# Optimization experiments

Measured on AMD Instinct MI355X. Metric: run time of the kernel, lower is better.

Reference implementation:

```python
import jax, jax.numpy as jnp
import numpy as np

PAD = 0

def setup_inputs() -> dict:
    key = jax.random.key(0)
    ks = jax.random.split(key, 16)
    B, S, D, F = 64, 512, 768, 256
    VOCAB = 32000
    # variable-length tweets: length in [8, S], rest is padding (token id PAD=0)
    lengths = jax.random.randint(ks[0], (B,), 8, S + 1)
    tok = jax.random.randint(ks[1], (B, S), 1, VOCAB)
    x = jnp.where(jnp.arange(S)[None, :] < lengths[:, None], tok, PAD)
    h = jax.random.normal(ks[2], (B, S, D), dtype=jnp.float32)
    sc = 0.02
    w2 = jax.random.normal(ks[3], (F, D, 2), dtype=jnp.float32) * sc
    b2 = jax.random.normal(ks[4], (F,), dtype=jnp.float32) * sc
    w3 = jax.random.normal(ks[5], (F, D, 3), dtype=jnp.float32) * sc
    b3 = jax.random.normal(ks[6], (F,), dtype=jnp.float32) * sc
    w4 = jax.random.normal(ks[7], (F, D, 4), dtype=jnp.float32) * sc
    b4 = jax.random.normal(ks[8], (F,), dtype=jnp.float32) * sc
    w5 = jax.random.normal(ks[9], (F, D, 5), dtype=jnp.float32) * sc
    b5 = jax.random.normal(ks[10], (F,), dtype=jnp.float32) * sc
    fc_w = jax.random.normal(ks[11], (1, 4 * F), dtype=jnp.float32) * sc
    fc_b = jax.random.normal(ks[12], (1,), dtype=jnp.float32) * sc
    return {"x": x, "h": h, "w2": w2, "b2": b2, "w3": w3, "b3": b3,
            "w4": w4, "b4": b4, "w5": w5, "b5": b5, "fc_w": fc_w, "fc_b": fc_b}


def _branch(hc, L, w, b):
    # hc: [B, D, S] front-compacted hidden states; w: [F, D, k]
    k = w.shape[-1]
    out = jax.lax.conv_general_dilated(
        hc, w, window_strides=(1,), padding='VALID',
        dimension_numbers=('NCH', 'OIH', 'NCH')) + b[None, :, None]  # [B,F,S-k+1]
    T = out.shape[-1]
    # conv position t is valid iff t + k - 1 < L  <=>  t < L - k + 1
    valid = jnp.arange(T)[None, :] < (L - k + 1)[:, None]           # [B,T]
    neg = jnp.asarray(-jnp.inf, out.dtype)
    pooled = jnp.max(jnp.where(valid[:, None, :], out, neg), axis=-1)  # [B,F]
    return jax.nn.relu(pooled)


def reference(x, h, w2, b2, w3, b3, w4, b4, w5, b5, fc_w, fc_b):
    mask = x != PAD                                   # [B,S]
    L = mask.sum(axis=1)                              # [B]
    # stable compaction: move non-pad token hidden states to the front, order preserved
    order = jnp.argsort(jnp.logical_not(mask), axis=1, stable=True)   # [B,S]
    hc = jnp.take_along_axis(h, order[..., None], axis=1)             # [B,S,D]
    hc = hc.transpose(0, 2, 1)                                        # [B,D,S]
    feats = jnp.concatenate([
        _branch(hc, L, w2, b2),
        _branch(hc, L, w3, b3),
        _branch(hc, L, w4, b4),
        _branch(hc, L, w5, b5),
    ], axis=-1)                                       # [B, 4F]
    logits = feats @ fc_w.T + fc_b                    # [B,1]
    return jax.nn.sigmoid(logits).squeeze(-1)         # [B]
```

## Files before the change

kernel.cpp:

```cpp
#include <hip/hip_runtime.h>
#include <stdint.h>

#define Bn 64
#define Sn 512
#define SPn 520
#define Dn 768
#define JSTRIDE 196608
#define ABUF 16640
#define BSLOT 8192
#define QS_A 28.222222f
#define SAQ 0.035433072f

typedef int iv4 __attribute__((ext_vector_type(4)));

static __device__ __forceinline__ signed char q8(float f, float s) {
  float t = __builtin_rintf(f * s);
  t = fmaxf(-127.f, fminf(127.f, t));
  return (signed char)(int)t;
}

static __device__ __forceinline__ void gload16(const void* g, void* l) {
  __builtin_amdgcn_global_load_lds(
      (const __attribute__((address_space(1))) unsigned int*)g,
      (__attribute__((address_space(3))) unsigned int*)l, 16, 0, 0);
}

template<int N> __device__ __forceinline__ void waitv() {
  static_assert(N == 0 || N == 1 || N == 4, "");
  if constexpr (N == 0) asm volatile("s_waitcnt vmcnt(0)" ::: "memory");
  else if constexpr (N == 1) asm volatile("s_waitcnt vmcnt(1)" ::: "memory");
  else asm volatile("s_waitcnt vmcnt(4)" ::: "memory");
}

__global__ __launch_bounds__(256) void plan_kernel(
    const int* __restrict__ x, int* __restrict__ plan, int* __restrict__ rowmap) {
  __shared__ int sL[64];
  __shared__ int sOff[65];
  int tid = threadIdx.x, lane = tid & 63, wv = tid >> 6;
  for (int bb = wv; bb < 64; bb += 4) {
    int cnt = 0;
    for (int c = 0; c < 8; ++c) {
      unsigned long long m = __ballot(x[bb * Sn + c * 64 + lane] != 0);
      cnt += __popcll(m);
    }
    if (lane == 0) sL[bb] = cnt;
  }
  __syncthreads();
  if (tid < 64) {
    int L = sL[tid];
    int SL = (L + 15) & ~15;
    int pre = SL;
    #pragma unroll
    for (int off = 1; off < 64; off <<= 1) {
      int y = __shfl_up(pre, off);
      if (tid >= off) pre += y;
    }
    sOff[tid] = pre - SL;
    if (tid == 63) { sOff[64] = pre; plan[0] = (pre + 255) >> 8; }
  }
  __syncthreads();
  int M = sOff[64];
  for (int b = 0; b < 64; ++b) {
    int off = sOff[b], L = sL[b];
    int SL = (L + 15) & ~15;
    int enc = (b << 20) | (L << 10);
    for (int t = tid; t < SL; t += 256) rowmap[off + t] = enc | t;
  }
  for (int p = M + tid; p < M + 264; p += 256)
    rowmap[p] = 512;
}

__global__ __launch_bounds__(256) void stage_kernel(
    const int* __restrict__ x, const float* __restrict__ h,
    const float* __restrict__ w2, const float* __restrict__ w3,
    const float* __restrict__ w4, const float* __restrict__ w5,
    signed char* __restrict__ hcq, signed char* __restrict__ wq,
    float* __restrict__ fscale) {
  int tid = threadIdx.x, lane = tid & 63, wv = tid >> 6;
  if (blockIdx.x < 512) {
    int cidx = blockIdx.x;
    int b = cidx >> 3, rblk = cidx & 7;
    __shared__ unsigned long long masks[8];
    __shared__ short sidx[Sn];
    for (int c = wv; c < 8; c += 4) {
      unsigned long long m = __ballot(x[b * Sn + c * 64 + lane] != 0);
      if (lane == 0) masks[c] = m;
    }
    __syncthreads();
    int pref[9]; pref[0] = 0;
    #pragma unroll
    for (int c = 0; c < 8; ++c) pref[c + 1] = pref[c] + __popcll(masks[c]);
    int L = pref[8];
    for (int p = tid; p < Sn; p += 256) {
      int c = p >> 6, l = p & 63;
      unsigned long long m = masks[c];
      if ((m >> l) & 1ull)
        sidx[pref[c] + __popcll(m & ((1ull << l) - 1ull))] = (short)p;
    }
    __syncthreads();
    int r0 = rblk * 65;
    for (int r = r0 + wv; r < r0 + 65; r += 4) {
      if (r < L) {
        signed char* dst = hcq + ((size_t)b * SPn + r) * Dn;
        const float* src = h + ((size_t)b * Sn + sidx[r]) * Dn;
        #pragma unroll
        for (int c = 0; c < 3; ++c) {
          int d = c * 256 + lane * 4;
          float4 v = *(const float4*)(src + d);
          char4 o = { q8(v.x, QS_A), q8(v.y, QS_A), q8(v.z, QS_A), q8(v.w, QS_A) };
          *(char4*)(dst + d) = o;
        }
      }
    }
  } else {
    __shared__ float sf[3840];
    __shared__ float smax[4];
    int bb = blockIdx.x - 512;
    int br = bb >> 8, f = bb & 255, k = br + 2;
    const float* w = (br == 0) ? w2 : (br == 1) ? w3 : (br == 2) ? w4 : w5;
    int mBase = 256 * ((br * (br + 3)) >> 1);
    const float* src = w + (size_t)f * Dn * k;
    int n = Dn * k;
    float mx = 0.f;
    for (int e = tid; e < n; e += 256) {
      float v = src[e];
      sf[e] = v;
      mx = fmaxf(mx, fabsf(v));
    }
    #pragma unroll
    for (int off = 32; off; off >>= 1) mx = fmaxf(mx, __shfl_xor(mx, off));
    if (lane == 0) smax[wv] = mx;
    __syncthreads();
    float M = fmaxf(fmaxf(smax[0], smax[1]), fmaxf(smax[2], smax[3]));
    M = fmaxf(M, 1e-30f);
    if (tid == 0) fscale[br * 256 + f] = M / 127.f;
    float qs = 127.f / M;
    for (int j = 0; j < k; ++j) {
      signed char* dst = wq + (size_t)(mBase + j * 256 + f) * Dn;
      for (int d = tid; d < Dn; d += 256) dst[d] = q8(sf[d * k + j], qs);
    }
  }
}

static __device__ __forceinline__ void issueA(
    int d0i, char* sA, const char* const (&gA)[2], const char* gAt,
    int lane, int wvoff) {
  int aoff = (d0i + 1) * 64;
  char* nA = sA + ((d0i + 1) & 1) * ABUF;
  #pragma unroll
  for (int p = 0; p < 2; ++p) gload16(gA[p] + aoff, nA + p * 8192 + wvoff);
  if (lane < 16) gload16(gAt + aoff, nA + 16384);
}

template<int J, int W, int J2, int DADD, int DOA>
static __device__ __forceinline__ void conv_step(
    int d0i, int bsl0, char* sA, char* sB,
    const char* const (&gA)[2], const char* gAt, const char* gB0,
    int lane, int wr, int wc, int lrow, int lg, int wvoff, iv4 (&acc)[4][4]) {
  int sl = bsl0 + J;      sl  -= (sl  >= 3) ? 3 : 0; sl  -= (sl  >= 3) ? 3 : 0;
  int dsl = bsl0 + J + 2; dsl -= (dsl >= 3) ? 3 : 0; dsl -= (dsl >= 3) ? 3 : 0;
  {
    int boff = J2 * JSTRIDE + (d0i + DADD) * 64;
    gload16(gB0 + boff, sB + dsl * BSLOT + wvoff);
  }
  if constexpr (DOA) issueA(d0i, sA, gA, gAt, lane, wvoff);
  const char* curA = sA + (d0i & 1) * ABUF;
  const char* curB = sB + sl * BSLOT;
  iv4 Af[4], Bf[4];
  #pragma unroll
  for (int m = 0; m < 4; ++m) {
    int row = wr * 64 + m * 16 + lrow + J;
    Af[m] = *(const iv4*)(curA + row * 64 + ((lg ^ ((row >> 1) & 3)) << 4));
  }
  #pragma unroll
  for (int n = 0; n < 4; ++n) {
    int row = wc * 64 + n * 16 + lrow;
    Bf[n] = *(const iv4*)(curB + row * 64 + ((lg ^ ((row >> 1) & 3)) << 4));
  }
  __builtin_amdgcn_s_setprio(1);
  #pragma unroll
  for (int n = 0; n < 4; ++n)
    #pragma unroll
    for (int m = 0; m < 4; ++m)
      acc[m][n] = __builtin_amdgcn_mfma_i32_16x16x64_i8(Af[m], Bf[n], acc[m][n], 0, 0, 0);
  __builtin_amdgcn_s_setprio(0);
  __builtin_amdgcn_sched_barrier(0);
  waitv<W>();
  __builtin_amdgcn_sched_barrier(0);
  __builtin_amdgcn_s_barrier();
  __builtin_amdgcn_sched_barrier(0);
}

#define SA bsl0, sA, sB, gA, gAt, gB0, lane, wr, wc, lrow, lg, wvoff, acc

template<int KK>
static __device__ __forceinline__ void conv_loop(
    char* sA, char* sB, const char* const (&gA)[2], const char* gAt,
    const char* gB0,
    int lane, int wr, int wc, int lrow, int lg, int wvoff, iv4 (&acc)[4][4]) {
  #pragma unroll
  for (int p = 0; p < 2; ++p) gload16(gA[p], sA + p * 8192 + wvoff);
  if (lane < 16) gload16(gAt, sA + 16384);
  gload16(gB0, sB + wvoff);
  gload16(gB0 + JSTRIDE, sB + BSLOT + wvoff);
  __builtin_amdgcn_sched_barrier(0);
  waitv<1>();
  __builtin_amdgcn_sched_barrier(0);
  __builtin_amdgcn_s_barrier();
  __builtin_amdgcn_sched_barrier(0);
  int bsl0 = 0;
  for (int d0i = 0; d0i < 11; ++d0i) {
    if constexpr (KK == 5) {
      conv_step<0,4,2,0,1>(d0i, SA);
      conv_step<1,4,3,0,0>(d0i, SA);
      conv_step<2,1,4,0,0>(d0i, SA);
      conv_step<3,1,0,1,0>(d0i, SA);
      conv_step<4,1,1,1,0>(d0i, SA);
    } else if constexpr (KK == 4) {
      conv_step<0,4,2,0,1>(d0i, SA);
      conv_step<1,4,3,0,0>(d0i, SA);
      conv_step<2,1,0,1,0>(d0i, SA);
      conv_step<3,1,1,1,0>(d0i, SA);
    } else if constexpr (KK == 3) {
      conv_step<0,4,2,0,1>(d0i, SA);
      conv_step<1,4,0,1,0>(d0i, SA);
      conv_step<2,1,1,1,0>(d0i, SA);
    } else {
      conv_step<0,4,0,1,1>(d0i, SA);
      conv_step<1,1,1,1,0>(d0i, SA);
    }
    bsl0 += KK; bsl0 -= (bsl0 >= 3) ? 3 : 0; bsl0 -= (bsl0 >= 3) ? 3 : 0;
  }
  if constexpr (KK == 5) {
    conv_step<0,1,2,0,0>(11, SA);
    conv_step<1,1,3,0,0>(11, SA);
    conv_step<2,1,4,0,0>(11, SA);
    conv_step<3,1,0,1,0>(11, SA);
    conv_step<4,1,1,1,0>(11, SA);
  } else if constexpr (KK == 4) {
    conv_step<0,1,2,0,0>(11, SA);
    conv_step<1,1,3,0,0>(11, SA);
    conv_step<2,1,0,1,0>(11, SA);
    conv_step<3,1,1,1,0>(11, SA);
  } else if constexpr (KK == 3) {
    conv_step<0,1,2,0,0>(11, SA);
    conv_step<1,1,0,1,0>(11, SA);
    conv_step<2,1,1,1,0>(11, SA);
  } else {
    conv_step<0,1,0,1,0>(11, SA);
    conv_step<1,1,1,1,0>(11, SA);
  }
  waitv<0>();
}

__global__ __launch_bounds__(512, 4) void conv_kernel(
    const signed char* __restrict__ hcq, const signed char* __restrict__ wq,
    const float* __restrict__ b2, const float* __restrict__ b3,
    const float* __restrict__ b4, const float* __restrict__ b5,
    const float* __restrict__ fscale,
    const int* __restrict__ plan, const int* __restrict__ rowmap,
    int* __restrict__ feats) {
  __shared__ char smem[2 * ABUF + 3 * BSLOT];
  char* sA = smem;
  char* sB = smem + 2 * ABUF;
  int idx = blockIdx.x;
  int xcd = idx & 7, s2 = idx >> 3;
  int sub = s2 & 7, tile = xcd + ((s2 >> 3) << 3);
  if (tile >= plan[0]) return;
  int br = 3 - (sub >> 1), ff = sub & 1, kk = br + 2;
  int mBase = 256 * ((br * (br + 3)) >> 1) + ff * 128;
  const float* bias = (br == 0) ? b2 : (br == 1) ? b3 : (br == 2) ? b4 : b5;
  int tid = threadIdx.x, lane = tid & 63, wv = tid >> 6;
  int wr = wv >> 1, wc = wv & 1;
  int lrow = lane & 15, lg = lane >> 4;
  int wvoff = wv * 1024;
  int P0 = tile << 8;

  const char* gA[2];
  #pragma unroll
  for (int p = 0; p < 2; ++p) {
    int c = p * 512 + tid;
    int row = c >> 2, sgp = c & 3;
    int rm = rowmap[P0 + row];
    int bb_ = rm >> 20, t = rm & 1023;
    int seg = sgp ^ ((row >> 1) & 3);
    gA[p] = (const char*)(hcq + ((size_t)(bb_ * SPn + t)) * Dn + seg * 16);
  }
  const char* gAt;
  {
    int l = lane & 15;
    int row = 256 + (l >> 2), sgp = l & 3;
    int rm = rowmap[P0 + row];
    int bb_ = rm >> 20, t = rm & 1023;
    int seg = sgp ^ ((row >> 1) & 3);
    gAt = (const char*)(hcq + ((size_t)(bb_ * SPn + t)) * Dn + seg * 16);
  }
  const char* gB0;
  {
    int row = tid >> 2, sgp = tid & 3;
    int seg = sgp ^ ((row >> 1) & 3);
    gB0 = (const char*)(wq + ((size_t)(mBase + row)) * Dn + seg * 16);
  }

  iv4 acc[4][4];
  #pragma unroll
  for (int m = 0; m < 4; ++m)
    #pragma unroll
    for (int n = 0; n < 4; ++n) acc[m][n] = (iv4)0;

  switch (br) {
    case 3: conv_loop<5>(sA, sB, gA, gAt, gB0, lane, wr, wc, lrow, lg, wvoff, acc); break;
    case 2: conv_loop<4>(sA, sB, gA, gAt, gB0, lane, wr, wc, lrow, lg, wvoff, acc); break;
    case 1: conv_loop<3>(sA, sB, gA, gAt, gB0, lane, wr, wc, lrow, lg, wvoff, acc); break;
    default: conv_loop<2>(sA, sB, gA, gAt, gB0, lane, wr, wc, lrow, lg, wvoff, acc); break;
  }

  int rmv[4];
  #pragma unroll
  for (int m = 0; m < 4; ++m) rmv[m] = rowmap[P0 + wr * 64 + m * 16];
  #pragma unroll
  for (int n = 0; n < 4; ++n) {
    int fg = ff * 128 + wc * 64 + n * 16 + lrow;
    float bv = bias[fg];
    float sfc = fscale[br * 256 + fg] * SAQ;
    #pragma unroll
    for (int m = 0; m < 4; ++m) {
      int bb_ = rmv[m] >> 20;
      int Lb = (rmv[m] >> 10) & 1023;
      int t0 = (rmv[m] & 1023) + lg * 4;
      int vlim = Lb - kk + 1;
      float pmax = 0.f;
      #pragma unroll
      for (int i = 0; i < 4; ++i) {
        float v = (float)acc[m][n][i] * sfc + bv;
        pmax = fmaxf(pmax, (t0 + i < vlim) ? fmaxf(v, 0.f) : 0.f);
      }
      pmax = fmaxf(pmax, __shfl_xor(pmax, 16));
      pmax = fmaxf(pmax, __shfl_xor(pmax, 32));
      if (lane < 16 && pmax > 0.f)
        atomicMax(feats + bb_ * 1024 + br * 256 + fg, __float_as_int(pmax));
    }
  }
}

__global__ __launch_bounds__(64) void fc_kernel(
    const int* __restrict__ feats, const float* __restrict__ fcw,
    const float* __restrict__ fcb, float* __restrict__ out) {
  int b = blockIdx.x, lane = threadIdx.x;
  float acc = 0.f;
  for (int i = lane; i < 1024; i += 64)
    acc += __int_as_float(feats[b * 1024 + i]) * fcw[i];
  #pragma unroll
  for (int off = 32; off; off >>= 1) acc += __shfl_xor(acc, off);
  if (lane == 0) out[b] = 1.f / (1.f + expf(-(acc + fcb[0])));
}

extern "C" void kernel_launch(void* const* d_in, const int* in_sizes, int n_in,
                              void* d_out, int out_size, void* d_ws, size_t ws_size,
                              hipStream_t stream) {
  const int*   x   = (const int*)d_in[0];
  const float* h   = (const float*)d_in[1];
  const float* w2  = (const float*)d_in[2];
  const float* b2  = (const float*)d_in[3];
  const float* w3  = (const float*)d_in[4];
  const float* b3  = (const float*)d_in[5];
  const float* w4  = (const float*)d_in[6];
  const float* b4  = (const float*)d_in[7];
  const float* w5  = (const float*)d_in[8];
  const float* b5  = (const float*)d_in[9];
  const float* fcw = (const float*)d_in[10];
  const float* fcb = (const float*)d_in[11];
  float* out = (float*)d_out;
  char* ws = (char*)d_ws;
  signed char* hcq = (signed char*)ws;
  signed char* wq  = (signed char*)(ws + 25559040);
  float* fscale = (float*)(ws + 28311552);
  int* feats  = (int*)(ws + 28315648);
  int* plan   = (int*)(ws + 28577792);
  int* rowmap = (int*)(ws + 28577808);

  hipMemsetAsync(feats, 0, 64 * 1024 * 4, stream);
  plan_kernel<<<1, 256, 0, stream>>>(x, plan, rowmap);
  stage_kernel<<<1536, 256, 0, stream>>>(x, h, w2, w3, w4, w5, hcq, wq, fscale);
  conv_kernel<<<1024, 512, 0, stream>>>(hcq, wq, b2, b3, b4, b5, fscale, plan, rowmap, feats);
  fc_kernel<<<64, 64, 0, stream>>>(feats, fcw, fcb, out);
}
```

Measured before the change: 115.2 us.

## Stage all conv taps per depth chunk with double buffering, fold memset into plan kernel

Replaces the per-tap fine-grained pipeline (three rotating B slots, one barrier per tap, explicit vmcnt waits) with a coarser double-buffered scheme. Each depth chunk now loads all KK weight taps plus the activation tile, then computes every tap, with one __syncthreads per chunk. This cuts barrier count, but LDS grows to roughly 115KB per block and the occupancy hint is dropped, so fewer blocks fit per CU and the prefetch relies on the compiler's implicit waits. It also zeroes feats inside plan_kernel instead of calling hipMemsetAsync, and vectorizes the weight-quantization stores to char4.

After: 110.0 us. 4.5% less time.

```diff
diff --git a/kernel.cpp b/kernel.cpp
--- a/kernel.cpp
+++ b/kernel.cpp
@@ -25,18 +25,16 @@
       (__attribute__((address_space(3))) unsigned int*)l, 16, 0, 0);
 }
 
-template<int N> __device__ __forceinline__ void waitv() {
-  static_assert(N == 0 || N == 1 || N == 4, "");
-  if constexpr (N == 0) asm volatile("s_waitcnt vmcnt(0)" ::: "memory");
-  else if constexpr (N == 1) asm volatile("s_waitcnt vmcnt(1)" ::: "memory");
-  else asm volatile("s_waitcnt vmcnt(4)" ::: "memory");
-}
-
 __global__ __launch_bounds__(256) void plan_kernel(
-    const int* __restrict__ x, int* __restrict__ plan, int* __restrict__ rowmap) {
+    const int* __restrict__ x, int* __restrict__ plan, int* __restrict__ rowmap,
+    int* __restrict__ feats) {
   __shared__ int sL[64];
   __shared__ int sOff[65];
   int tid = threadIdx.x, lane = tid & 63, wv = tid >> 6;
+  {
+    int4 z = {0, 0, 0, 0};
+    for (int i = tid * 4; i < 65536; i += 1024) *(int4*)(feats + i) = z;
+  }
   for (int bb = wv; bb < 64; bb += 4) {
     int cnt = 0;
     for (int c = 0; c < 8; ++c) {
@@ -137,130 +135,86 @@
     float qs = 127.f / M;
     for (int j = 0; j < k; ++j) {
       signed char* dst = wq + (size_t)(mBase + j * 256 + f) * Dn;
-      for (int d = tid; d < Dn; d += 256) dst[d] = q8(sf[d * k + j], qs);
-    }
-  }
-}
-
-static __device__ __forceinline__ void issueA(
-    int d0i, char* sA, const char* const (&gA)[2], const char* gAt,
-    int lane, int wvoff) {
-  int aoff = (d0i + 1) * 64;
-  char* nA = sA + ((d0i + 1) & 1) * ABUF;
-  #pragma unroll
-  for (int p = 0; p < 2; ++p) gload16(gA[p] + aoff, nA + p * 8192 + wvoff);
-  if (lane < 16) gload16(gAt + aoff, nA + 16384);
-}
-
-template<int J, int W, int J2, int DADD, int DOA>
-static __device__ __forceinline__ void conv_step(
-    int d0i, int bsl0, char* sA, char* sB,
-    const char* const (&gA)[2], const char* gAt, const char* gB0,
-    int lane, int wr, int wc, int lrow, int lg, int wvoff, iv4 (&acc)[4][4]) {
-  int sl = bsl0 + J;      sl  -= (sl  >= 3) ? 3 : 0; sl  -= (sl  >= 3) ? 3 : 0;
-  int dsl = bsl0 + J + 2; dsl -= (dsl >= 3) ? 3 : 0; dsl -= (dsl >= 3) ? 3 : 0;
-  {
-    int boff = J2 * JSTRIDE + (d0i + DADD) * 64;
-    gload16(gB0 + boff, sB + dsl * BSLOT + wvoff);
-  }
-  if constexpr (DOA) issueA(d0i, sA, gA, gAt, lane, wvoff);
-  const char* curA = sA + (d0i & 1) * ABUF;
-  const char* curB = sB + sl * BSLOT;
-  iv4 Af[4], Bf[4];
-  #pragma unroll
-  for (int m = 0; m < 4; ++m) {
-    int row = wr * 64 + m * 16 + lrow + J;
-    Af[m] = *(const iv4*)(curA + row * 64 + ((lg ^ ((row >> 1) & 3)) << 4));
-  }
-  #pragma unroll
-  for (int n = 0; n < 4; ++n) {
-    int row = wc * 64 + n * 16 + lrow;
-    Bf[n] = *(const iv4*)(curB + row * 64 + ((lg ^ ((row >> 1) & 3)) << 4));
-  }
-  __builtin_amdgcn_s_setprio(1);
-  #pragma unroll
-  for (int n = 0; n < 4; ++n)
-    #pragma unroll
-    for (int m = 0; m < 4; ++m)
-      acc[m][n] = __builtin_amdgcn_mfma_i32_16x16x64_i8(Af[m], Bf[n], acc[m][n], 0, 0, 0);
-  __builtin_amdgcn_s_setprio(0);
-  __builtin_amdgcn_sched_barrier(0);
-  waitv<W>();
-  __builtin_amdgcn_sched_barrier(0);
-  __builtin_amdgcn_s_barrier();
-  __builtin_amdgcn_sched_barrier(0);
-}
-
-#define SA bsl0, sA, sB, gA, gAt, gB0, lane, wr, wc, lrow, lg, wvoff, acc
+      for (int d4 = tid * 4; d4 < Dn; d4 += 1024) {
+        char4 o = { q8(sf[(d4 + 0) * k + j], qs), q8(sf[(d4 + 1) * k + j], qs),
+                    q8(sf[(d4 + 2) * k + j], qs), q8(sf[(d4 + 3) * k + j], qs) };
+        *(char4*)(dst + d4) = o;
+      }
+    }
+  }
+}
+
+template<int KK>
+static __device__ __forceinline__ void stageAll(
+    int d0, char* sA, char* sB, const char* const (&gA)[2], const char* gAt,
+    const char* gB0, int lane, int wvoff) {
+  int buf = d0 & 1;
+  char* bB = sB + buf * (KK * BSLOT);
+  int doff = d0 * 64;
+  #pragma unroll
+  for (int tap = 0; tap < KK; ++tap)
+    gload16(gB0 + tap * JSTRIDE + doff, bB + tap * BSLOT + wvoff);
+  char* nA = sA + buf * ABUF;
+  gload16(gA[0] + doff, nA + wvoff);
+  gload16(gA[1] + doff, nA + 8192 + wvoff);
+  if (lane < 16) gload16(gAt + doff, nA + 16384);
+}
+
+template<int KK>
+static __device__ __forceinline__ void computeD0(
+    int d0, const char* sA, const char* sB, int wr, int wc, int lrow, int lg,
+    iv4 (&acc)[4][4]) {
+  int buf = d0 & 1;
+  const char* curA = sA + buf * ABUF;
+  const char* bB = sB + buf * (KK * BSLOT);
+  #pragma unroll
+  for (int j = 0; j < KK; ++j) {
+    const char* curB = bB + j * BSLOT;
+    iv4 Af[4], Bf[4];
+    #pragma unroll
+    for (int n = 0; n < 4; ++n) {
+      int row = wc * 64 + n * 16 + lrow;
+      Bf[n] = *(const iv4*)(curB + row * 64 + ((lg ^ ((row >> 1) & 3)) << 4));
+    }
+    #pragma unroll
+    for (int m = 0; m < 4; ++m) {
+      int row = wr * 64 + m * 16 + lrow + j;
+      Af[m] = *(const iv4*)(curA + row * 64 + ((lg ^ ((row >> 1) & 3)) << 4));
+    }
+    __builtin_amdgcn_s_setprio(1);
+    #pragma unroll
+    for (int n = 0; n < 4; ++n)
+      #pragma unroll
+      for (int m = 0; m < 4; ++m)
+        acc[m][n] = __builtin_amdgcn_mfma_i32_16x16x64_i8(Af[m], Bf[n], acc[m][n], 0, 0, 0);
+    __builtin_amdgcn_s_setprio(0);
+  }
+}
 
 template<int KK>
 static __device__ __forceinline__ void conv_loop(
     char* sA, char* sB, const char* const (&gA)[2], const char* gAt,
-    const char* gB0,
-    int lane, int wr, int wc, int lrow, int lg, int wvoff, iv4 (&acc)[4][4]) {
-  #pragma unroll
-  for (int p = 0; p < 2; ++p) gload16(gA[p], sA + p * 8192 + wvoff);
-  if (lane < 16) gload16(gAt, sA + 16384);
-  gload16(gB0, sB + wvoff);
-  gload16(gB0 + JSTRIDE, sB + BSLOT + wvoff);
-  __builtin_amdgcn_sched_barrier(0);
-  waitv<1>();
-  __builtin_amdgcn_sched_barrier(0);
-  __builtin_amdgcn_s_barrier();
-  __builtin_amdgcn_sched_barrier(0);
-  int bsl0 = 0;
-  for (int d0i = 0; d0i < 11; ++d0i) {
-    if constexpr (KK == 5) {
-      conv_step<0,4,2,0,1>(d0i, SA);
-      conv_step<1,4,3,0,0>(d0i, SA);
-      conv_step<2,1,4,0,0>(d0i, SA);
-      conv_step<3,1,0,1,0>(d0i, SA);
-      conv_step<4,1,1,1,0>(d0i, SA);
-    } else if constexpr (KK == 4) {
-      conv_step<0,4,2,0,1>(d0i, SA);
-      conv_step<1,4,3,0,0>(d0i, SA);
-      conv_step<2,1,0,1,0>(d0i, SA);
-      conv_step<3,1,1,1,0>(d0i, SA);
-    } else if constexpr (KK == 3) {
-      conv_step<0,4,2,0,1>(d0i, SA);
-      conv_step<1,4,0,1,0>(d0i, SA);
-      conv_step<2,1,1,1,0>(d0i, SA);
-    } else {
-      conv_step<0,4,0,1,1>(d0i, SA);
-      conv_step<1,1,1,1,0>(d0i, SA);
-    }
-    bsl0 += KK; bsl0 -= (bsl0 >= 3) ? 3 : 0; bsl0 -= (bsl0 >= 3) ? 3 : 0;
-  }
-  if constexpr (KK == 5) {
-    conv_step<0,1,2,0,0>(11, SA);
-    conv_step<1,1,3,0,0>(11, SA);
-    conv_step<2,1,4,0,0>(11, SA);
-    conv_step<3,1,0,1,0>(11, SA);
-    conv_step<4,1,1,1,0>(11, SA);
-  } else if constexpr (KK == 4) {
-    conv_step<0,1,2,0,0>(11, SA);
-    conv_step<1,1,3,0,0>(11, SA);
-    conv_step<2,1,0,1,0>(11, SA);
-    conv_step<3,1,1,1,0>(11, SA);
-  } else if constexpr (KK == 3) {
-    conv_step<0,1,2,0,0>(11, SA);
-    conv_step<1,1,0,1,0>(11, SA);
-    conv_step<2,1,1,1,0>(11, SA);
-  } else {
-    conv_step<0,1,0,1,0>(11, SA);
-    conv_step<1,1,1,1,0>(11, SA);
-  }
-  waitv<0>();
-}
-
-__global__ __launch_bounds__(512, 4) void conv_kernel(
+    const char* gB0, int lane, int wr, int wc, int lrow, int lg, int wvoff,
+    iv4 (&acc)[4][4]) {
+  stageAll<KK>(0, sA, sB, gA, gAt, gB0, lane, wvoff);
+  __syncthreads();
+  #pragma unroll 2
+  for (int d0 = 0; d0 < 11; ++d0) {
+    stageAll<KK>(d0 + 1, sA, sB, gA, gAt, gB0, lane, wvoff);
+    computeD0<KK>(d0, sA, sB, wr, wc, lrow, lg, acc);
+    __syncthreads();
+  }
+  computeD0<KK>(11, sA, sB, wr, wc, lrow, lg, acc);
+}
+
+__global__ __launch_bounds__(512) void conv_kernel(
     const signed char* __restrict__ hcq, const signed char* __restrict__ wq,
     const float* __restrict__ b2, const float* __restrict__ b3,
     const float* __restrict__ b4, const float* __restrict__ b5,
     const float* __restrict__ fscale,
     const int* __restrict__ plan, const int* __restrict__ rowmap,
     int* __restrict__ feats) {
-  __shared__ char smem[2 * ABUF + 3 * BSLOT];
+  __shared__ char smem[2 * ABUF + 2 * 5 * BSLOT];
   char* sA = smem;
   char* sB = smem + 2 * ABUF;
   int idx = blockIdx.x;
@@ -379,8 +333,7 @@
   int* plan   = (int*)(ws + 28577792);
   int* rowmap = (int*)(ws + 28577808);
 
-  hipMemsetAsync(feats, 0, 64 * 1024 * 4, stream);
-  plan_kernel<<<1, 256, 0, stream>>>(x, plan, rowmap);
+  plan_kernel<<<1, 256, 0, stream>>>(x, plan, rowmap, feats);
   stage_kernel<<<1536, 256, 0, stream>>>(x, h, w2, w3, w4, w5, hcq, wq, fscale);
   conv_kernel<<<1024, 512, 0, stream>>>(hcq, wq, b2, b3, b4, b5, fscale, plan, rowmap, feats);
   fc_kernel<<<64, 64, 0, stream>>>(feats, fcw, fcb, out);
```
